# Kernel optimization log

Hardware: AMD Instinct MI355X
Metric: run time of the kernel (lower is better)

The kernel has to match this reference:

```python
import jax, jax.numpy as jnp
import numpy as np

N = 500_000          # number of tree nodes
K = 8                # attributes per group
ROWS, COLS = 2048, 4096   # image size; P = ROWS*COLS pixels


def _build_euler_tour(n, seed=0):
    """Random tree (parent[i] < i, parent[0] = 0) + real DFS Euler tour with a
    single timer incremented on both entry (tpre) and exit (tpost)."""
    rng = np.random.default_rng(seed)
    parent = np.zeros(n, dtype=np.int64)
    if n > 1:
        parent[1:] = np.floor(rng.random(n - 1) * np.arange(1, n)).astype(np.int64)
    counts = np.bincount(parent[1:], minlength=n)
    starts = np.zeros(n, dtype=np.int64)
    starts[1:] = np.cumsum(counts)[:-1]
    child_order = np.argsort(parent[1:], kind='stable') + 1  # children grouped by parent
    tpre = np.empty(n, dtype=np.int64)
    tpost = np.empty(n, dtype=np.int64)
    next_child = starts.copy()
    ends = starts + counts
    stack = np.empty(n, dtype=np.int64)
    sp = 0
    stack[0] = 0
    timer = 0
    tpre[0] = timer; timer += 1
    while sp >= 0:
        u = stack[sp]
        if next_child[u] < ends[u]:
            v = child_order[next_child[u]]
            next_child[u] += 1
            sp += 1
            stack[sp] = v
            tpre[v] = timer; timer += 1
        else:
            tpost[u] = timer; timer += 1
            sp -= 1
    return tpre, tpost


def setup_inputs() -> dict:
    key = jax.random.key(0)
    k1, k2, k3, k4 = jax.random.split(key, 4)
    tpre_np, tpost_np = _build_euler_tour(N)
    weight = jax.random.normal(k1, (K,), dtype=jnp.float32) * 0.1
    bias = jnp.zeros((1,), dtype=jnp.float32)
    residues = jax.random.normal(k2, (N,), dtype=jnp.float32)
    attrs2d = jax.random.uniform(k3, (N, K), dtype=jnp.float32)
    node_of_pixel = jax.random.randint(k4, (ROWS * COLS,), 0, N)
    return {
        'weight': weight,
        'bias': bias,
        'residues': residues,
        'attrs2d': attrs2d,
        'tpre': jnp.asarray(tpre_np),
        'tpost': jnp.asarray(tpost_np),
        'node_of_pixel': node_of_pixel,
        'numRows': ROWS,
        'numCols': COLS,
    }


def reference(weight, bias, residues, attrs2d, tpre, tpost, node_of_pixel, numRows, numCols):
    beta_f = 1.0  # module default; clamp_logits=False
    # logits = attrs2d @ w + b ; filtered residues per node
    logits = attrs2d @ weight + bias[0]                     # (N,)
    sig = jax.nn.sigmoid(beta_f * logits)                   # (N,)
    filtered = residues * sig                                # (N,)
    # implicit J.T @ filtered via Euler-tour scatter + prefix scan
    T = 2 * tpre.shape[0]                                    # tpost.max()+1 for a full DFS tour
    delta = (jnp.zeros((T,), dtype=filtered.dtype)
             .at[tpre].add(filtered)
             .at[tpost].add(-filtered))
    y_cumsum = jnp.cumsum(delta)                             # (2N,)
    y = y_cumsum[tpre[node_of_pixel]]                        # (P,) gather per pixel
    return y.reshape(numRows, numCols)
```

## Files before the change

### kernel.cpp

```cpp
#include <hip/hip_runtime.h>

#define SCAN_THREADS 256
#define EPT 8
#define CHUNK (SCAN_THREADS * EPT)

typedef int   v4i __attribute__((ext_vector_type(4)));
typedef float v4f __attribute__((ext_vector_type(4)));

__global__ void k1_filter_scatter(const float* __restrict__ attrs,
                                  const float* __restrict__ weight,
                                  const float* __restrict__ bias,
                                  const float* __restrict__ residues,
                                  const int* __restrict__ tpre,
                                  const int* __restrict__ tpost,
                                  float* __restrict__ delta,
                                  int N) {
    int u0 = (blockIdx.x * blockDim.x + threadIdx.x) * 2;
    v4f w0 = *(const v4f*)weight;
    v4f w1 = *(const v4f*)(weight + 4);
    float b = bias[0];
    if (u0 + 2 <= N) {
        float r0 = residues[u0], r1 = residues[u0 + 1];
        int pre0 = tpre[u0],  pre1 = tpre[u0 + 1];
        int pos0 = tpost[u0], pos1 = tpost[u0 + 1];
        v4f a00 = *(const v4f*)(attrs + (size_t)u0 * 8);
        v4f a01 = *(const v4f*)(attrs + (size_t)u0 * 8 + 4);
        v4f a10 = *(const v4f*)(attrs + (size_t)u0 * 8 + 8);
        v4f a11 = *(const v4f*)(attrs + (size_t)u0 * 8 + 12);
        float l0 = a00.x*w0.x + a00.y*w0.y + a00.z*w0.z + a00.w*w0.w +
                   a01.x*w1.x + a01.y*w1.y + a01.z*w1.z + a01.w*w1.w + b;
        float l1 = a10.x*w0.x + a10.y*w0.y + a10.z*w0.z + a10.w*w0.w +
                   a11.x*w1.x + a11.y*w1.y + a11.z*w1.z + a11.w*w1.w + b;
        float f0 = r0 / (1.0f + __expf(-l0));
        float f1 = r1 / (1.0f + __expf(-l1));
        delta[pre0] =  f0; delta[pre1] =  f1;
        delta[pos0] = -f0; delta[pos1] = -f1;
    } else {
        for (int u = u0; u < N; ++u) {
            float logit = b;
            #pragma unroll
            for (int k = 0; k < 8; ++k) logit += attrs[(size_t)u * 8 + k] * weight[k];
            float f = residues[u] / (1.0f + __expf(-logit));
            delta[tpre[u]]  =  f;
            delta[tpost[u]] = -f;
        }
    }
}

__global__ void k2_partials(const float* __restrict__ delta,
                            float* __restrict__ partials, int T) {
    __shared__ float sdata[SCAN_THREADS / 64];
    int base = blockIdx.x * CHUNK + threadIdx.x * EPT;
    float s = 0.0f;
    if (base + EPT <= T) {
        v4f v0 = *(const v4f*)(delta + base);
        v4f v1 = *(const v4f*)(delta + base + 4);
        s = v0.x + v0.y + v0.z + v0.w + v1.x + v1.y + v1.z + v1.w;
    } else {
        for (int i = 0; i < EPT; ++i)
            if (base + i < T) s += delta[base + i];
    }
    #pragma unroll
    for (int d = 32; d > 0; d >>= 1) s += __shfl_down(s, d, 64);
    int lane = threadIdx.x & 63, wid = threadIdx.x >> 6;
    if (lane == 0) sdata[wid] = s;
    __syncthreads();
    if (threadIdx.x == 0)
        partials[blockIdx.x] = sdata[0] + sdata[1] + sdata[2] + sdata[3];
}

__global__ void k4_scan_chunks(float* __restrict__ data,
                               const float* __restrict__ partials, int T) {
    __shared__ float wavesums[SCAN_THREADS / 64];
    __shared__ float redsum[SCAN_THREADS / 64];
    int lane = threadIdx.x & 63, wid = threadIdx.x >> 6;

    float c = 0.0f;
    for (int i = threadIdx.x; i < blockIdx.x; i += SCAN_THREADS)
        c += partials[i];
    #pragma unroll
    for (int d = 32; d > 0; d >>= 1) c += __shfl_down(c, d, 64);
    if (lane == 0) redsum[wid] = c;

    int base = blockIdx.x * CHUNK + threadIdx.x * EPT;
    float v[EPT];
    bool full = (base + EPT <= T);
    if (full) {
        v4f v0 = *(const v4f*)(data + base);
        v4f v1 = *(const v4f*)(data + base + 4);
        v[0]=v0.x; v[1]=v0.y; v[2]=v0.z; v[3]=v0.w;
        v[4]=v1.x; v[5]=v1.y; v[6]=v1.z; v[7]=v1.w;
    } else {
        for (int i = 0; i < EPT; ++i)
            v[i] = (base + i < T) ? data[base + i] : 0.0f;
    }
    float run = 0.0f;
    #pragma unroll
    for (int i = 0; i < EPT; ++i) { run += v[i]; v[i] = run; }
    float tot = run;
    float x = tot;
    #pragma unroll
    for (int d = 1; d < 64; d <<= 1) {
        float y = __shfl_up(x, d, 64);
        if (lane >= d) x += y;
    }
    if (lane == 63) wavesums[wid] = x;
    __syncthreads();
    float woff = 0.0f, offset = redsum[0] + redsum[1] + redsum[2] + redsum[3];
    #pragma unroll
    for (int i = 0; i < SCAN_THREADS / 64; ++i)
        if (i < wid) woff += wavesums[i];
    float add = (x - tot) + woff + offset;
    if (full) {
        v4f o0 = { v[0]+add, v[1]+add, v[2]+add, v[3]+add };
        v4f o1 = { v[4]+add, v[5]+add, v[6]+add, v[7]+add };
        *(v4f*)(data + base)     = o0;
        *(v4f*)(data + base + 4) = o1;
    } else {
        for (int i = 0; i < EPT; ++i)
            if (base + i < T) data[base + i] = v[i] + add;
    }
}

__global__ void k5_node_values(const float* __restrict__ ycum,
                               const int* __restrict__ tpre,
                               float* __restrict__ vnode, int N) {
    int u0 = (blockIdx.x * blockDim.x + threadIdx.x) * 2;
    if (u0 + 2 <= N) {
        int t0 = tpre[u0], t1 = tpre[u0 + 1];
        float y0 = ycum[t0], y1 = ycum[t1];
        vnode[u0] = y0; vnode[u0 + 1] = y1;
    } else {
        for (int u = u0; u < N; ++u) vnode[u] = ycum[tpre[u]];
    }
}

__global__ void k6_gather(const float* __restrict__ vnode,
                          const int* __restrict__ nop,
                          float* __restrict__ out, int P) {
    int i = (blockIdx.x * blockDim.x + threadIdx.x) * 8;
    if (i + 8 <= P) {
        v4i n0 = *(const v4i*)(nop + i);
        v4i n1 = *(const v4i*)(nop + i + 4);
        v4f o0 = { vnode[n0.x], vnode[n0.y], vnode[n0.z], vnode[n0.w] };
        v4f o1 = { vnode[n1.x], vnode[n1.y], vnode[n1.z], vnode[n1.w] };
        *(v4f*)(out + i)     = o0;
        *(v4f*)(out + i + 4) = o1;
    } else {
        for (; i < P; ++i) out[i] = vnode[nop[i]];
    }
}

__global__ void k6_direct(const float* __restrict__ ycum,
                          const int* __restrict__ tpre,
                          const int* __restrict__ nop,
                          float* __restrict__ out, int P) {
    int i = (blockIdx.x * blockDim.x + threadIdx.x) * 4;
    if (i + 4 <= P) {
        v4i n = *(const v4i*)(nop + i);
        v4f o = { ycum[tpre[n.x]], ycum[tpre[n.y]], ycum[tpre[n.z]], ycum[tpre[n.w]] };
        *(v4f*)(out + i) = o;
    } else {
        for (; i < P; ++i) out[i] = ycum[tpre[nop[i]]];
    }
}

extern "C" void kernel_launch(void* const* d_in, const int* in_sizes, int n_in,
                              void* d_out, int out_size, void* d_ws, size_t ws_size,
                              hipStream_t stream) {
    const float* weight   = (const float*)d_in[0];
    const float* bias     = (const float*)d_in[1];
    const float* residues = (const float*)d_in[2];
    const float* attrs    = (const float*)d_in[3];
    const int*   tpre     = (const int*)d_in[4];
    const int*   tpost    = (const int*)d_in[5];
    const int*   nop      = (const int*)d_in[6];
    float* out = (float*)d_out;

    const int N = in_sizes[2];
    const int T = 2 * N;
    const int P = out_size;
    const int numChunks = (T + CHUNK - 1) / CHUNK;

    size_t needFull = (size_t)(T + N + 1024) * sizeof(float);
    size_t needMid  = (size_t)(N + 1024) * sizeof(float);

    float* delta;
    float* vnode    = nullptr;
    float* partials;
    bool useVnode = true;

    if (ws_size >= needFull) {
        delta    = (float*)d_ws;
        vnode    = delta + T;
        partials = vnode + N;
    } else if (ws_size >= needMid) {
        delta    = out;
        vnode    = (float*)d_ws;
        partials = vnode + N;
    } else {
        delta    = out;
        partials = (float*)d_ws;
        useVnode = false;
    }

    k1_filter_scatter<<<(N / 2 + 255) / 256, 256, 0, stream>>>(
        attrs, weight, bias, residues, tpre, tpost, delta, N);
    k2_partials<<<numChunks, SCAN_THREADS, 0, stream>>>(delta, partials, T);
    k4_scan_chunks<<<numChunks, SCAN_THREADS, 0, stream>>>(delta, partials, T);

    if (useVnode) {
        k5_node_values<<<(N / 2 + 255) / 256, 256, 0, stream>>>(delta, tpre, vnode, N);
        int gatherBlocks = (P / 8 + 255) / 256;
        k6_gather<<<gatherBlocks, 256, 0, stream>>>(vnode, nop, out, P);
    } else {
        int gatherBlocks = (P / 4 + 255) / 256;
        k6_direct<<<gatherBlocks, 256, 0, stream>>>(delta, tpre, nop, out, P);
    }
}
```

Before: 165.5 us.

## Fuse scan, node-value and gather stages into one cooperative persistent kernel

Replaces the partials, chunk-scan, node-value and pixel-gather launches with a single cooperative kernel of 1024 persistent blocks that separates phases with grid-wide syncs. The gather phase becomes grid-stride and uses nontemporal loads of node indices and nontemporal stores of the output. The goal is to remove per-launch overhead and the idle gaps between dependent kernels. In exchange it adds three grid barriers and limits parallelism in the gather phase to the co-resident grid size.

```diff
diff --git a/kernel.cpp b/kernel.cpp
--- a/kernel.cpp
+++ b/kernel.cpp
@@ -1,8 +1,12 @@
 #include <hip/hip_runtime.h>
+#include <hip/hip_cooperative_groups.h>
+
+namespace cg = cooperative_groups;
 
 #define SCAN_THREADS 256
 #define EPT 8
 #define CHUNK (SCAN_THREADS * EPT)
+#define COOP_BLOCKS 1024
 
 typedef int   v4i __attribute__((ext_vector_type(4)));
 typedef float v4f __attribute__((ext_vector_type(4)));
@@ -47,6 +51,118 @@
     }
 }
 
+__global__ __launch_bounds__(SCAN_THREADS, 4)
+void k_fused(float* __restrict__ delta,
+             float* __restrict__ partials,
+             float* __restrict__ vnode,
+             const int* __restrict__ tpre,
+             const int* __restrict__ nop,
+             float* __restrict__ out,
+             int N, int T, int P, int numChunks)
+{
+    cg::grid_group grid = cg::this_grid();
+    __shared__ float smem[8];
+    const int tid  = threadIdx.x;
+    const int lane = tid & 63, wid = tid >> 6;
+
+    for (int cch = blockIdx.x; cch < numChunks; cch += gridDim.x) {
+        int base = cch * CHUNK + tid * EPT;
+        float s = 0.0f;
+        if (base + EPT <= T) {
+            v4f v0 = *(const v4f*)(delta + base);
+            v4f v1 = *(const v4f*)(delta + base + 4);
+            s = v0.x + v0.y + v0.z + v0.w + v1.x + v1.y + v1.z + v1.w;
+        } else {
+            for (int i = 0; i < EPT; ++i)
+                if (base + i < T) s += delta[base + i];
+        }
+        #pragma unroll
+        for (int d = 32; d > 0; d >>= 1) s += __shfl_down(s, d, 64);
+        if (lane == 0) smem[wid] = s;
+        __syncthreads();
+        if (tid == 0) partials[cch] = smem[0] + smem[1] + smem[2] + smem[3];
+        __syncthreads();
+    }
+    grid.sync();
+
+    for (int cch = blockIdx.x; cch < numChunks; cch += gridDim.x) {
+        float c = 0.0f;
+        for (int i = tid; i < cch; i += SCAN_THREADS) c += partials[i];
+        #pragma unroll
+        for (int d = 32; d > 0; d >>= 1) c += __shfl_down(c, d, 64);
+        if (lane == 0) smem[4 + wid] = c;
+
+        int base = cch * CHUNK + tid * EPT;
+        float v[EPT];
+        bool full = (base + EPT <= T);
+        if (full) {
+            v4f v0 = *(const v4f*)(delta + base);
+            v4f v1 = *(const v4f*)(delta + base + 4);
+            v[0]=v0.x; v[1]=v0.y; v[2]=v0.z; v[3]=v0.w;
+            v[4]=v1.x; v[5]=v1.y; v[6]=v1.z; v[7]=v1.w;
+        } else {
+            for (int i = 0; i < EPT; ++i)
+                v[i] = (base + i < T) ? delta[base + i] : 0.0f;
+        }
+        float run = 0.0f;
+        #pragma unroll
+        for (int i = 0; i < EPT; ++i) { run += v[i]; v[i] = run; }
+        float tot = run;
+        float x = tot;
+        #pragma unroll
+        for (int d = 1; d < 64; d <<= 1) {
+            float y = __shfl_up(x, d, 64);
+            if (lane >= d) x += y;
+        }
+        if (lane == 63) smem[wid] = x;
+        __syncthreads();
+        float woff = 0.0f, offset = smem[4] + smem[5] + smem[6] + smem[7];
+        #pragma unroll
+        for (int i = 0; i < SCAN_THREADS / 64; ++i)
+            if (i < wid) woff += smem[i];
+        float add = (x - tot) + woff + offset;
+        if (full) {
+            v4f o0 = { v[0]+add, v[1]+add, v[2]+add, v[3]+add };
+            v4f o1 = { v[4]+add, v[5]+add, v[6]+add, v[7]+add };
+            *(v4f*)(delta + base)     = o0;
+            *(v4f*)(delta + base + 4) = o1;
+        } else {
+            for (int i = 0; i < EPT; ++i)
+                if (base + i < T) delta[base + i] = v[i] + add;
+        }
+        __syncthreads();
+    }
+    grid.sync();
+
+    {
+        int u0 = (blockIdx.x * SCAN_THREADS + tid) * 2;
+        if (u0 + 2 <= N) {
+            int t0 = tpre[u0], t1 = tpre[u0 + 1];
+            float y0 = delta[t0], y1 = delta[t1];
+            vnode[u0] = y0; vnode[u0 + 1] = y1;
+        } else {
+            for (int u = u0; u < N; ++u) vnode[u] = delta[tpre[u]];
+        }
+    }
+    grid.sync();
+
+    {
+        const int stride8 = gridDim.x * SCAN_THREADS * 8;
+        for (int i = (blockIdx.x * SCAN_THREADS + tid) * 8; i < P; i += stride8) {
+            if (i + 8 <= P) {
+                v4i n0 = __builtin_nontemporal_load((const v4i*)(nop + i));
+                v4i n1 = __builtin_nontemporal_load((const v4i*)(nop + i + 4));
+                v4f o0 = { vnode[n0.x], vnode[n0.y], vnode[n0.z], vnode[n0.w] };
+                v4f o1 = { vnode[n1.x], vnode[n1.y], vnode[n1.z], vnode[n1.w] };
+                __builtin_nontemporal_store(o0, (v4f*)(out + i));
+                __builtin_nontemporal_store(o1, (v4f*)(out + i + 4));
+            } else {
+                for (int j = i; j < P; ++j) out[j] = vnode[nop[j]];
+            }
+        }
+    }
+}
+
 __global__ void k2_partials(const float* __restrict__ delta,
                             float* __restrict__ partials, int T) {
     __shared__ float sdata[SCAN_THREADS / 64];
@@ -74,7 +190,6 @@
     __shared__ float wavesums[SCAN_THREADS / 64];
     __shared__ float redsum[SCAN_THREADS / 64];
     int lane = threadIdx.x & 63, wid = threadIdx.x >> 6;
-
     float c = 0.0f;
     for (int i = threadIdx.x; i < blockIdx.x; i += SCAN_THREADS)
         c += partials[i];
@@ -119,35 +234,6 @@
     } else {
         for (int i = 0; i < EPT; ++i)
             if (base + i < T) data[base + i] = v[i] + add;
-    }
-}
-
-__global__ void k5_node_values(const float* __restrict__ ycum,
-                               const int* __restrict__ tpre,
-                               float* __restrict__ vnode, int N) {
-    int u0 = (blockIdx.x * blockDim.x + threadIdx.x) * 2;
-    if (u0 + 2 <= N) {
-        int t0 = tpre[u0], t1 = tpre[u0 + 1];
-        float y0 = ycum[t0], y1 = ycum[t1];
-        vnode[u0] = y0; vnode[u0 + 1] = y1;
-    } else {
-        for (int u = u0; u < N; ++u) vnode[u] = ycum[tpre[u]];
-    }
-}
-
-__global__ void k6_gather(const float* __restrict__ vnode,
-                          const int* __restrict__ nop,
-                          float* __restrict__ out, int P) {
-    int i = (blockIdx.x * blockDim.x + threadIdx.x) * 8;
-    if (i + 8 <= P) {
-        v4i n0 = *(const v4i*)(nop + i);
-        v4i n1 = *(const v4i*)(nop + i + 4);
-        v4f o0 = { vnode[n0.x], vnode[n0.y], vnode[n0.z], vnode[n0.w] };
-        v4f o1 = { vnode[n1.x], vnode[n1.y], vnode[n1.z], vnode[n1.w] };
-        *(v4f*)(out + i)     = o0;
-        *(v4f*)(out + i + 4) = o1;
-    } else {
-        for (; i < P; ++i) out[i] = vnode[nop[i]];
     }
 }
 
@@ -188,32 +274,42 @@
     float* delta;
     float* vnode    = nullptr;
     float* partials;
-    bool useVnode = true;
+    int tier;
 
     if (ws_size >= needFull) {
         delta    = (float*)d_ws;
         vnode    = delta + T;
         partials = vnode + N;
+        tier = 2;
     } else if (ws_size >= needMid) {
         delta    = out;
         vnode    = (float*)d_ws;
         partials = vnode + N;
+        tier = 1;
     } else {
         delta    = out;
         partials = (float*)d_ws;
-        useVnode = false;
+        tier = 0;
     }
 
     k1_filter_scatter<<<(N / 2 + 255) / 256, 256, 0, stream>>>(
         attrs, weight, bias, residues, tpre, tpost, delta, N);
-    k2_partials<<<numChunks, SCAN_THREADS, 0, stream>>>(delta, partials, T);
-    k4_scan_chunks<<<numChunks, SCAN_THREADS, 0, stream>>>(delta, partials, T);
-
-    if (useVnode) {
-        k5_node_values<<<(N / 2 + 255) / 256, 256, 0, stream>>>(delta, tpre, vnode, N);
-        int gatherBlocks = (P / 8 + 255) / 256;
-        k6_gather<<<gatherBlocks, 256, 0, stream>>>(vnode, nop, out, P);
-    } else {
+
+    if (tier >= 1) {
+        float* deltaArg = delta;
+        float* partialsArg = partials;
+        float* vnodeArg = vnode;
+        const int* tpreArg = tpre;
+        const int* nopArg = nop;
+        float* outArg = out;
+        int nN = N, nT = T, nP = P, nC = numChunks;
+        void* args[] = { &deltaArg, &partialsArg, &vnodeArg, &tpreArg, &nopArg,
+                         &outArg, &nN, &nT, &nP, &nC };
+        hipLaunchCooperativeKernel(k_fused, dim3(COOP_BLOCKS), dim3(SCAN_THREADS),
+                                   args, 0, stream);
+    } else {
+        k2_partials<<<numChunks, SCAN_THREADS, 0, stream>>>(delta, partials, T);
+        k4_scan_chunks<<<numChunks, SCAN_THREADS, 0, stream>>>(delta, partials, T);
         int gatherBlocks = (P / 4 + 255) / 256;
         k6_direct<<<gatherBlocks, 256, 0, stream>>>(delta, tpre, nop, out, P);
     }
```

After: 473.7 us. +186.2%, slower.

## Fuse chunk partial sums into scatter kernel via shared-memory histogram

Applied to the files above, without the earlier changes.

The scatter kernel now builds a per-block histogram of chunk sums in LDS with atomics and flushes it to global partials. This removes the separate k2 reduction pass over delta when the chunk count fits. In exchange it adds a memset launch, many LDS atomics and up to ~490 global atomics per block. Separately, streaming inputs and the output switch to nontemporal loads and stores, and k5 is widened to four nodes per thread.

```diff
diff --git a/kernel.cpp b/kernel.cpp
--- a/kernel.cpp
+++ b/kernel.cpp
@@ -3,9 +3,68 @@
 #define SCAN_THREADS 256
 #define EPT 8
 #define CHUNK (SCAN_THREADS * EPT)
-
+#define CHUNK_SHIFT 11
+#define MAX_CHUNKS 1024
+
+typedef int   v2i __attribute__((ext_vector_type(2)));
 typedef int   v4i __attribute__((ext_vector_type(4)));
+typedef float v2f __attribute__((ext_vector_type(2)));
 typedef float v4f __attribute__((ext_vector_type(4)));
+
+__global__ void k1_filter_scatter_hist(const float* __restrict__ attrs,
+                                       const float* __restrict__ weight,
+                                       const float* __restrict__ bias,
+                                       const float* __restrict__ residues,
+                                       const int* __restrict__ tpre,
+                                       const int* __restrict__ tpost,
+                                       float* __restrict__ delta,
+                                       float* __restrict__ partials,
+                                       int N, int numChunks) {
+    __shared__ float hist[MAX_CHUNKS];
+    for (int i = threadIdx.x; i < numChunks; i += SCAN_THREADS) hist[i] = 0.0f;
+    __syncthreads();
+
+    int u0 = (blockIdx.x * blockDim.x + threadIdx.x) * 2;
+    v4f w0 = *(const v4f*)weight;
+    v4f w1 = *(const v4f*)(weight + 4);
+    float b = bias[0];
+    if (u0 + 2 <= N) {
+        v2f rr = __builtin_nontemporal_load((const v2f*)(residues + u0));
+        v2i pr = __builtin_nontemporal_load((const v2i*)(tpre + u0));
+        v2i po = __builtin_nontemporal_load((const v2i*)(tpost + u0));
+        v4f a00 = __builtin_nontemporal_load((const v4f*)(attrs + (size_t)u0 * 8));
+        v4f a01 = __builtin_nontemporal_load((const v4f*)(attrs + (size_t)u0 * 8 + 4));
+        v4f a10 = __builtin_nontemporal_load((const v4f*)(attrs + (size_t)u0 * 8 + 8));
+        v4f a11 = __builtin_nontemporal_load((const v4f*)(attrs + (size_t)u0 * 8 + 12));
+        float l0 = a00.x*w0.x + a00.y*w0.y + a00.z*w0.z + a00.w*w0.w +
+                   a01.x*w1.x + a01.y*w1.y + a01.z*w1.z + a01.w*w1.w + b;
+        float l1 = a10.x*w0.x + a10.y*w0.y + a10.z*w0.z + a10.w*w0.w +
+                   a11.x*w1.x + a11.y*w1.y + a11.z*w1.z + a11.w*w1.w + b;
+        float f0 = rr.x / (1.0f + __expf(-l0));
+        float f1 = rr.y / (1.0f + __expf(-l1));
+        delta[pr.x] =  f0; delta[pr.y] =  f1;
+        delta[po.x] = -f0; delta[po.y] = -f1;
+        atomicAdd(&hist[pr.x >> CHUNK_SHIFT],  f0);
+        atomicAdd(&hist[pr.y >> CHUNK_SHIFT],  f1);
+        atomicAdd(&hist[po.x >> CHUNK_SHIFT], -f0);
+        atomicAdd(&hist[po.y >> CHUNK_SHIFT], -f1);
+    } else {
+        for (int u = u0; u < N; ++u) {
+            float logit = b;
+            #pragma unroll
+            for (int k = 0; k < 8; ++k) logit += attrs[(size_t)u * 8 + k] * weight[k];
+            float f = residues[u] / (1.0f + __expf(-logit));
+            int pre = tpre[u], pos = tpost[u];
+            delta[pre] =  f;
+            delta[pos] = -f;
+            atomicAdd(&hist[pre >> CHUNK_SHIFT],  f);
+            atomicAdd(&hist[pos >> CHUNK_SHIFT], -f);
+        }
+    }
+    __syncthreads();
+    for (int i = threadIdx.x; i < numChunks; i += SCAN_THREADS)
+        atomicAdd(&partials[i], hist[i]);
+}
 
 __global__ void k1_filter_scatter(const float* __restrict__ attrs,
                                   const float* __restrict__ weight,
@@ -20,9 +79,9 @@
     v4f w1 = *(const v4f*)(weight + 4);
     float b = bias[0];
     if (u0 + 2 <= N) {
-        float r0 = residues[u0], r1 = residues[u0 + 1];
-        int pre0 = tpre[u0],  pre1 = tpre[u0 + 1];
-        int pos0 = tpost[u0], pos1 = tpost[u0 + 1];
+        v2f rr = *(const v2f*)(residues + u0);
+        v2i pr = *(const v2i*)(tpre + u0);
+        v2i po = *(const v2i*)(tpost + u0);
         v4f a00 = *(const v4f*)(attrs + (size_t)u0 * 8);
         v4f a01 = *(const v4f*)(attrs + (size_t)u0 * 8 + 4);
         v4f a10 = *(const v4f*)(attrs + (size_t)u0 * 8 + 8);
@@ -31,10 +90,10 @@
                    a01.x*w1.x + a01.y*w1.y + a01.z*w1.z + a01.w*w1.w + b;
         float l1 = a10.x*w0.x + a10.y*w0.y + a10.z*w0.z + a10.w*w0.w +
                    a11.x*w1.x + a11.y*w1.y + a11.z*w1.z + a11.w*w1.w + b;
-        float f0 = r0 / (1.0f + __expf(-l0));
-        float f1 = r1 / (1.0f + __expf(-l1));
-        delta[pre0] =  f0; delta[pre1] =  f1;
-        delta[pos0] = -f0; delta[pos1] = -f1;
+        float f0 = rr.x / (1.0f + __expf(-l0));
+        float f1 = rr.y / (1.0f + __expf(-l1));
+        delta[pr.x] =  f0; delta[pr.y] =  f1;
+        delta[po.x] = -f0; delta[po.y] = -f1;
     } else {
         for (int u = u0; u < N; ++u) {
             float logit = b;
@@ -125,11 +184,11 @@
 __global__ void k5_node_values(const float* __restrict__ ycum,
                                const int* __restrict__ tpre,
                                float* __restrict__ vnode, int N) {
-    int u0 = (blockIdx.x * blockDim.x + threadIdx.x) * 2;
-    if (u0 + 2 <= N) {
-        int t0 = tpre[u0], t1 = tpre[u0 + 1];
-        float y0 = ycum[t0], y1 = ycum[t1];
-        vnode[u0] = y0; vnode[u0 + 1] = y1;
+    int u0 = (blockIdx.x * blockDim.x + threadIdx.x) * 4;
+    if (u0 + 4 <= N) {
+        v4i t = __builtin_nontemporal_load((const v4i*)(tpre + u0));
+        v4f y = { ycum[t.x], ycum[t.y], ycum[t.z], ycum[t.w] };
+        *(v4f*)(vnode + u0) = y;
     } else {
         for (int u = u0; u < N; ++u) vnode[u] = ycum[tpre[u]];
     }
@@ -140,12 +199,12 @@
                           float* __restrict__ out, int P) {
     int i = (blockIdx.x * blockDim.x + threadIdx.x) * 8;
     if (i + 8 <= P) {
-        v4i n0 = *(const v4i*)(nop + i);
-        v4i n1 = *(const v4i*)(nop + i + 4);
+        v4i n0 = __builtin_nontemporal_load((const v4i*)(nop + i));
+        v4i n1 = __builtin_nontemporal_load((const v4i*)(nop + i + 4));
         v4f o0 = { vnode[n0.x], vnode[n0.y], vnode[n0.z], vnode[n0.w] };
         v4f o1 = { vnode[n1.x], vnode[n1.y], vnode[n1.z], vnode[n1.w] };
-        *(v4f*)(out + i)     = o0;
-        *(v4f*)(out + i + 4) = o1;
+        __builtin_nontemporal_store(o0, (v4f*)(out + i));
+        __builtin_nontemporal_store(o1, (v4f*)(out + i + 4));
     } else {
         for (; i < P; ++i) out[i] = vnode[nop[i]];
     }
@@ -204,13 +263,22 @@
         useVnode = false;
     }
 
-    k1_filter_scatter<<<(N / 2 + 255) / 256, 256, 0, stream>>>(
-        attrs, weight, bias, residues, tpre, tpost, delta, N);
-    k2_partials<<<numChunks, SCAN_THREADS, 0, stream>>>(delta, partials, T);
+    const int k1Blocks = (N / 2 + 255) / 256;
+
+    if (numChunks <= MAX_CHUNKS) {
+        (void)hipMemsetAsync(partials, 0, (size_t)numChunks * sizeof(float), stream);
+        k1_filter_scatter_hist<<<k1Blocks, 256, 0, stream>>>(
+            attrs, weight, bias, residues, tpre, tpost, delta, partials, N, numChunks);
+    } else {
+        k1_filter_scatter<<<k1Blocks, 256, 0, stream>>>(
+            attrs, weight, bias, residues, tpre, tpost, delta, N);
+        k2_partials<<<numChunks, SCAN_THREADS, 0, stream>>>(delta, partials, T);
+    }
+
     k4_scan_chunks<<<numChunks, SCAN_THREADS, 0, stream>>>(delta, partials, T);
 
     if (useVnode) {
-        k5_node_values<<<(N / 2 + 255) / 256, 256, 0, stream>>>(delta, tpre, vnode, N);
+        k5_node_values<<<(N / 4 + 255) / 256, 256, 0, stream>>>(delta, tpre, vnode, N);
         int gatherBlocks = (P / 8 + 255) / 256;
         k6_gather<<<gatherBlocks, 256, 0, stream>>>(vnode, nop, out, P);
     } else {
```

Result: slower. 188.3 us (+13.8%).
